# Optimization experiments

Hardware: AMD Instinct MI355X
Metric: run time of the kernel (lower is better)

The kernel has to match this reference:

```python
import jax, jax.numpy as jnp
import numpy as np

D_MODEL = 1024
NHEADS = 16
D_K = D_MODEL // NHEADS


def setup_inputs() -> dict:
    key = jax.random.key(0)
    ks = jax.random.split(key, 5)
    s = 1.0 / np.sqrt(D_MODEL)
    x = jax.random.normal(ks[0], (4, 2048, D_MODEL), dtype=jnp.float32)
    Wq = jax.random.normal(ks[1], (D_MODEL, D_MODEL), dtype=jnp.float32) * s
    Wk = jax.random.normal(ks[2], (D_MODEL, D_MODEL), dtype=jnp.float32) * s
    Wv = jax.random.normal(ks[3], (D_MODEL, D_MODEL), dtype=jnp.float32) * s
    Wo = jax.random.normal(ks[4], (D_MODEL, D_MODEL), dtype=jnp.float32) * s
    z = jnp.zeros((D_MODEL,), dtype=jnp.float32)
    return {"x": x, "Wq": Wq, "bq": z, "Wk": Wk, "bk": z,
            "Wv": Wv, "bv": z, "Wo": Wo, "bo": z}


def reference(x, Wq, bq, Wk, bk, Wv, bv, Wo, bo):
    B, S, _ = x.shape
    # nn.Linear: y = x @ W^T + b  (weights stored [out, in])
    def proj(W, b):
        h = x @ W.T + b                       # [B, S, D]
        return h.reshape(B, S, NHEADS, D_K).transpose(0, 2, 1, 3)  # [B, H, S, d_k]
    Q = proj(Wq, bq)
    K = proj(Wk, bk)
    V = proj(Wv, bv)
    scores = jnp.einsum("bhqd,bhkd->bhqk", Q, K) / jnp.sqrt(jnp.float32(D_K))
    attn = jax.nn.softmax(scores, axis=-1)    # dropout p=0.0 -> identity
    ctx = jnp.einsum("bhqk,bhkd->bhqd", attn, V)
    ctx = ctx.transpose(0, 2, 1, 3).reshape(B, S, D_MODEL)
    return ctx @ Wo.T + bo
```

## Files before the change

kernel.cpp:

```cpp
#include <hip/hip_runtime.h>
#include <stdint.h>
#include <stddef.h>

typedef _Float16 f16;
typedef f16 f16x8 __attribute__((ext_vector_type(8)));
typedef f16 f16x4 __attribute__((ext_vector_type(4)));
typedef f16 f16x2 __attribute__((ext_vector_type(2)));
typedef float f32x4 __attribute__((ext_vector_type(4)));
typedef float f32x16 __attribute__((ext_vector_type(16)));
typedef unsigned int u32x4 __attribute__((ext_vector_type(4)));

#define SEQ 2048
#define DM 1024
#define NH 16
#define DK 64
#define MTOT 8192

__device__ __forceinline__ void gload16(const f16* g, f16* l) {
    __builtin_amdgcn_global_load_lds(
        (const __attribute__((address_space(1))) uint32_t*)g,
        (__attribute__((address_space(3))) uint32_t*)l,
        16, 0, 0);
}

__device__ __forceinline__ unsigned int pkrtz(float a, float b) {
    return __builtin_bit_cast(unsigned int, __builtin_amdgcn_cvt_pkrtz(a, b));
}

__device__ __forceinline__ void plswap(unsigned int& a, unsigned int& b) {
    auto r = __builtin_amdgcn_permlane32_swap(a, b, false, false);
    unsigned int n0 = r[0], n1 = r[1];
    a = n0; b = n1;
}
__device__ __forceinline__ float xhalf_sum(float x) {
    unsigned int ux = __builtin_bit_cast(unsigned int, x);
    auto r = __builtin_amdgcn_permlane32_swap(ux, ux, false, false);
    unsigned int n0 = r[0], n1 = r[1];
    return __builtin_bit_cast(float, n0) + __builtin_bit_cast(float, n1);
}

__global__ void cvt_all(const float* __restrict__ x,
                        const float* __restrict__ w0, const float* __restrict__ w1,
                        const float* __restrict__ w2, const float* __restrict__ w3,
                        f16* __restrict__ xh,
                        f16* __restrict__ d0, f16* __restrict__ d1,
                        f16* __restrict__ d2, f16* __restrict__ d3) {
    int bid = blockIdx.x;
    const float* s;
    f16* d;
    int off;
    if (bid < 4096) { s = x; d = xh; off = bid; }
    else {
        int t = bid - 4096;
        int which = t >> 9;
        off = t & 511;
        s = which == 0 ? w0 : which == 1 ? w1 : which == 2 ? w2 : w3;
        d = which == 0 ? d0 : which == 1 ? d1 : which == 2 ? d2 : d3;
    }
    int i = (off * 256 + threadIdx.x) * 8;
    float4 a = *(const float4*)(s + i);
    float4 b = *(const float4*)(s + i + 4);
    f16x8 o = {(f16)a.x, (f16)a.y, (f16)a.z, (f16)a.w,
               (f16)b.x, (f16)b.y, (f16)b.z, (f16)b.w};
    *(f16x8*)(d + i) = o;
}

__device__ __forceinline__
void gemm_body(const f16* __restrict__ A, const f16* __restrict__ Bw,
               const float* __restrict__ bias, void* __restrict__ outp,
               int mode, float oscale, int bm, int bn, f16* As, f16* Bs) {
    const int tid = threadIdx.x;
    const int w = tid >> 6, lane = tid & 63;
    const int g = lane >> 4, c16 = lane & 15;
    const int wr = w >> 1, wc = w & 1;
    const int r8 = lane >> 3, co = (lane & 7) * 8;

    f32x4 acc[4][4] = {};

    const f16* Ab = A + (size_t)bm * 128 * DM;
    const f16* Bb = Bw + (size_t)bn * 128 * DM;

    for (int kt = 0; kt < DM / 64; ++kt) {
        if (kt) __syncthreads();
        const f16* As_src = Ab + kt * 64;
        const f16* Bs_src = Bb + kt * 64;
#pragma unroll
        for (int i = 0; i < 4; ++i) {
            int c = 4 * w + i;
            gload16(As_src + (size_t)(c * 8 + r8) * DM + co, As + c * 512);
            gload16(Bs_src + (size_t)(c * 8 + r8) * DM + co, Bs + c * 512);
        }
        __syncthreads();
#pragma unroll
        for (int kk = 0; kk < 2; ++kk) {
            f16x8 a[4], b[4];
            const int ko = kk * 32 + g * 8;
#pragma unroll
            for (int m = 0; m < 4; ++m)
                a[m] = *(const f16x8*)(As + (wr * 64 + m * 16 + c16) * 64 + ko);
#pragma unroll
            for (int n = 0; n < 4; ++n)
                b[n] = *(const f16x8*)(Bs + (wc * 64 + n * 16 + c16) * 64 + ko);
#pragma unroll
            for (int m = 0; m < 4; ++m)
#pragma unroll
                for (int n = 0; n < 4; ++n)
                    acc[m][n] = __builtin_amdgcn_mfma_f32_16x16x32_f16(a[m], b[n], acc[m][n], 0, 0, 0);
        }
    }

#pragma unroll
    for (int m = 0; m < 4; ++m) {
#pragma unroll
        for (int n = 0; n < 4; ++n) {
            const int col = bn * 128 + wc * 64 + n * 16 + c16;
            const float bv = bias[col];
            const int row0 = bm * 128 + wr * 64 + m * 16 + g * 4;
            if (mode == 1) {
                int b = row0 >> 11, s0 = row0 & 2047;
                int h = col >> 6, d = col & 63;
                f16x4 pv;
#pragma unroll
                for (int j = 0; j < 4; ++j) pv[j] = (f16)((acc[m][n][j] + bv) * oscale);
                *(f16x4*)((f16*)outp + (((size_t)(b * NH + h) * DK + d) * SEQ + s0)) = pv;
            } else if (mode == 0) {
#pragma unroll
                for (int j = 0; j < 4; ++j) {
                    int row = row0 + j;
                    int b = row >> 11, s = row & 2047;
                    int h = col >> 6, d = col & 63;
                    ((f16*)outp)[((size_t)(b * NH + h) * SEQ + s) * DK + d] =
                        (f16)((acc[m][n][j] + bv) * oscale);
                }
            } else {
#pragma unroll
                for (int j = 0; j < 4; ++j) {
                    int row = row0 + j;
                    ((float*)outp)[(size_t)row * DM + col] = acc[m][n][j] + bv;
                }
            }
        }
    }
}

__global__ __launch_bounds__(256, 2)
void gemm_qkv(const f16* __restrict__ A,
              const f16* __restrict__ W0, const f16* __restrict__ W1, const f16* __restrict__ W2,
              const float* __restrict__ b0, const float* __restrict__ b1, const float* __restrict__ b2,
              f16* __restrict__ Qo, f16* __restrict__ Ko, f16* __restrict__ Vto) {
    __shared__ __align__(16) f16 As[128 * 64];
    __shared__ __align__(16) f16 Bs[128 * 64];
    const int bid = blockIdx.x;
    const int wg = (bid & 7) * 192 + (bid >> 3);
    const int which = wg >> 9;
    const int t = wg & 511;
    const f16* Bw = which == 0 ? W0 : which == 1 ? W1 : W2;
    const float* bias = which == 0 ? b0 : which == 1 ? b1 : b2;
    void* outp = which == 0 ? (void*)Qo : which == 1 ? (void*)Ko : (void*)Vto;
    const int mode = (which == 2) ? 1 : 0;
    const float oscale = (which == 0) ? 0.18033688f : 1.0f;
    gemm_body(A, Bw, bias, outp, mode, oscale, t >> 3, t & 7, As, Bs);
}

__global__ __launch_bounds__(256, 2)
void gemm_out(const f16* __restrict__ A, const f16* __restrict__ Wo,
              const float* __restrict__ bias, float* __restrict__ outp) {
    __shared__ __align__(16) f16 As[128 * 64];
    __shared__ __align__(16) f16 Bs[128 * 64];
    const int bid = blockIdx.x;
    const int wg = (bid & 7) * 64 + (bid >> 3);
    gemm_body(A, Wo, bias, outp, 2, 1.0f, wg >> 3, wg & 7, As, Bs);
}

__global__ __launch_bounds__(512, 1)
void attn(const f16* __restrict__ Qg, const f16* __restrict__ Kg,
          const f16* __restrict__ Vg, f16* __restrict__ ctx) {
    __shared__ __align__(16) f16 SM[4][2][64 * 64];
    const int tid = threadIdx.x;
    const int w = tid >> 6, lane = tid & 63;
    const int q31 = lane & 31, hi = lane >> 5;
    const int bid = blockIdx.x;
    const int wg = (bid & 7) * 32 + (bid >> 3);
    const int bh = wg >> 2, qt = wg & 3;
    const int b = bh >> 4, h = bh & 15;
    const f16* Qp = Qg + (size_t)bh * SEQ * DK;
    const f16* Kp = Kg + (size_t)bh * SEQ * DK;
    const f16* Vp = Vg + (size_t)bh * DK * SEQ;
    const int q0w = qt * 512 + w * 64;

    f16x8 qfA[4], qfB[4];
#pragma unroll
    for (int ks4 = 0; ks4 < 4; ++ks4) {
        qfA[ks4] = *(const f16x8*)(Qp + (size_t)(q0w + q31) * DK + ks4 * 16 + hi * 8);
        qfB[ks4] = *(const f16x8*)(Qp + (size_t)(q0w + 32 + q31) * DK + ks4 * 16 + hi * 8);
    }

    const f32x16 z = {};
    const f16x2 one2 = {(f16)1.0f, (f16)1.0f};
    f32x16 OA0 = {}, OA1 = {}, OB0 = {}, OB1 = {};
    float lrA = 0.f, lrB = 0.f;

    const int srow = lane >> 3;
    const int scol = lane & 7;
    const int fsw = (q31 & 7) << 4;

#define STAGE(bufi, kvoff)                                                        \
    {                                                                             \
        int row_ = w * 8 + srow;                                                  \
        int csw_ = (scol ^ (row_ & 7)) * 8;                                       \
        gload16(Kp + (size_t)((kvoff) + row_) * DK + csw_, &SM[bufi][0][w * 512]); \
        gload16(Vp + (size_t)row_ * SEQ + (kvoff) + csw_, &SM[bufi][1][w * 512]);  \
    }

    auto qk = [&](const char* Kb, f32x16& A0, f32x16& A1, f32x16& B0, f32x16& B1) {
#pragma unroll
        for (int ks4 = 0; ks4 < 4; ++ks4) {
            const int off = (ks4 * 32 + hi * 16) ^ fsw;
            f16x8 kf0 = *(const f16x8*)(Kb + q31 * 128 + off);
            f16x8 kf1 = *(const f16x8*)(Kb + (32 + q31) * 128 + off);
            if (ks4 == 0) {
                A0 = __builtin_amdgcn_mfma_f32_32x32x16_f16(kf0, qfA[0], z, 0, 0, 0);
                B0 = __builtin_amdgcn_mfma_f32_32x32x16_f16(kf0, qfB[0], z, 0, 0, 0);
                A1 = __builtin_amdgcn_mfma_f32_32x32x16_f16(kf1, qfA[0], z, 0, 0, 0);
                B1 = __builtin_amdgcn_mfma_f32_32x32x16_f16(kf1, qfB[0], z, 0, 0, 0);
            } else {
                A0 = __builtin_amdgcn_mfma_f32_32x32x16_f16(kf0, qfA[ks4], A0, 0, 0, 0);
                B0 = __builtin_amdgcn_mfma_f32_32x32x16_f16(kf0, qfB[ks4], B0, 0, 0, 0);
                A1 = __builtin_amdgcn_mfma_f32_32x32x16_f16(kf1, qfA[ks4], A1, 0, 0, 0);
                B1 = __builtin_amdgcn_mfma_f32_32x32x16_f16(kf1, qfB[ks4], B1, 0, 0, 0);
            }
        }
    };

    auto pv = [&](const char* Vb, f16x8 (&pA)[4], f16x8 (&pB)[4]) {
#pragma unroll
        for (int ksl = 0; ksl < 4; ++ksl) {
            const int off = (ksl * 32 + hi * 16) ^ fsw;
            f16x8 vf0 = *(const f16x8*)(Vb + q31 * 128 + off);
            f16x8 vf1 = *(const f16x8*)(Vb + (32 + q31) * 128 + off);
            OA0 = __builtin_amdgcn_mfma_f32_32x32x16_f16(vf0, pA[ksl], OA0, 0, 0, 0);
            OA1 = __builtin_amdgcn_mfma_f32_32x32x16_f16(vf1, pA[ksl], OA1, 0, 0, 0);
            OB0 = __builtin_amdgcn_mfma_f32_32x32x16_f16(vf0, pB[ksl], OB0, 0, 0, 0);
            OB1 = __builtin_amdgcn_mfma_f32_32x32x16_f16(vf1, pB[ksl], OB1, 0, 0, 0);
        }
    };

    auto soft32 = [&](f32x16& sp, f16x8& paLo, f16x8& paHi, float& ls) {
#pragma unroll
        for (int r = 0; r < 16; ++r) sp[r] = __builtin_amdgcn_exp2f(sp[r]);
        unsigned int u[8];
#pragma unroll
        for (int j = 0; j < 4; ++j) {
            u[2 * j]     = pkrtz(sp[4 * j], sp[4 * j + 1]);
            u[2 * j + 1] = pkrtz(sp[4 * j + 2], sp[4 * j + 3]);
        }
        float ls0 = 0.f, ls1 = 0.f;
#pragma unroll
        for (int j = 0; j < 4; ++j) {
            ls0 = __builtin_amdgcn_fdot2(__builtin_bit_cast(f16x2, u[2 * j]), one2, ls0, false);
            ls1 = __builtin_amdgcn_fdot2(__builtin_bit_cast(f16x2, u[2 * j + 1]), one2, ls1, false);
        }
        ls += ls0 + ls1;
        plswap(u[0], u[2]);
        plswap(u[1], u[3]);
        plswap(u[4], u[6]);
        plswap(u[5], u[7]);
        u32x4 t0w = {u[0], u[1], u[2], u[3]};
        u32x4 t1w = {u[4], u[5], u[6], u[7]};
        paLo = __builtin_bit_cast(f16x8, t0w);
        paHi = __builtin_bit_cast(f16x8, t1w);
    };

    auto body = [&](int t, f16x8 (&pPA)[4], f16x8 (&pPB)[4],
                           f16x8 (&pCA)[4], f16x8 (&pCB)[4]) {
        if (t + 1 < 32) {
            asm volatile("s_waitcnt vmcnt(2)" ::: "memory");
        } else {
            asm volatile("s_waitcnt vmcnt(0)" ::: "memory");
        }
        __builtin_amdgcn_s_barrier();
        if (t + 2 < 32) STAGE((t + 2) & 3, (t + 2) * 64);

        const char* Kb = (const char*)&SM[t & 3][0][0];
        f32x16 sA0, sA1, sB0, sB1;
        if ((w >> 2) == 0) {
            qk(Kb, sA0, sA1, sB0, sB1);
            float lsA = 0.f, lsB = 0.f;
            soft32(sA0, pCA[0], pCA[1], lsA);
            soft32(sB0, pCB[0], pCB[1], lsB);
            soft32(sA1, pCA[2], pCA[3], lsA);
            soft32(sB1, pCB[2], pCB[3], lsB);
            lrA += lsA; lrB += lsB;
            pv((const char*)&SM[t & 3][1][0], pCA, pCB);
        } else {
            if (t > 0) pv((const char*)&SM[(t - 1) & 3][1][0], pPA, pPB);
            qk(Kb, sA0, sA1, sB0, sB1);
            float lsA = 0.f, lsB = 0.f;
            soft32(sA0, pCA[0], pCA[1], lsA);
            soft32(sB0, pCB[0], pCB[1], lsB);
            soft32(sA1, pCA[2], pCA[3], lsA);
            soft32(sB1, pCB[2], pCB[3], lsB);
            lrA += lsA; lrB += lsB;
        }
    };

    STAGE(0, 0);
    STAGE(1, 64);

    f16x8 paEA[4], paEB[4], paOA[4], paOB[4];
#pragma unroll
    for (int i = 0; i < 4; ++i) {
        paOA[i] = (f16x8){};
        paOB[i] = (f16x8){};
    }

    for (int t = 0; t < 32; t += 2) {
        body(t,     paOA, paOB, paEA, paEB);
        body(t + 1, paEA, paEB, paOA, paOB);
    }
    if ((w >> 2) != 0) {
        pv((const char*)&SM[3][1][0], paOA, paOB);
    }
#undef STAGE

    __syncthreads();

    f16* tw = &SM[0][0][0] + w * 4096;
    {
        const float rlA = 1.f / xhalf_sum(lrA);
        const float rlB = 1.f / xhalf_sum(lrB);
#pragma unroll
        for (int f = 0; f < 2; ++f) {
            const float rl = f ? rlB : rlA;
            char* twf = (char*)tw + f * 4096;
#pragma unroll
            for (int dblk = 0; dblk < 2; ++dblk) {
                const f32x16& Op = f ? (dblk ? OB1 : OB0) : (dblk ? OA1 : OA0);
#pragma unroll
                for (int rp = 0; rp < 8; ++rp) {
                    int r = 2 * rp;
                    int d0 = dblk * 32 + (r & 3) + 8 * (r >> 2) + 4 * hi;
                    unsigned int uv = pkrtz(Op[r] * rl, Op[r + 1] * rl);
                    *(unsigned int*)(twf + q31 * 128 + ((d0 * 2) ^ ((q31 & 7) << 4))) = uv;
                }
            }
        }
    }
#pragma unroll
    for (int p4 = 0; p4 < 8; ++p4) {
        int qq = p4 * 8 + (lane >> 3), ch = lane & 7;
        f16x8 v = *(const f16x8*)((const char*)tw + (qq >> 5) * 4096 + (qq & 31) * 128 +
                                  ((ch * 16) ^ ((qq & 7) << 4)));
        *(f16x8*)(ctx + (size_t)(b * SEQ + q0w + qq) * DM + h * DK + ch * 8) = v;
    }
}

extern "C" void kernel_launch(void* const* d_in, const int* in_sizes, int n_in,
                              void* d_out, int out_size, void* d_ws, size_t ws_size,
                              hipStream_t stream) {
    const float* x  = (const float*)d_in[0];
    const float* Wq = (const float*)d_in[1];
    const float* bq = (const float*)d_in[2];
    const float* Wk = (const float*)d_in[3];
    const float* bk = (const float*)d_in[4];
    const float* Wv = (const float*)d_in[5];
    const float* bv = (const float*)d_in[6];
    const float* Wo = (const float*)d_in[7];
    const float* bo = (const float*)d_in[8];

    f16* ws  = (f16*)d_ws;
    f16* xh  = ws;
    f16* Wqh = ws + (size_t)8 * 1024 * 1024;
    f16* Wkh = Wqh + 1024 * 1024;
    f16* Wvh = Wkh + 1024 * 1024;
    f16* Woh = Wvh + 1024 * 1024;
    f16* Vtb = Woh + 1024 * 1024;
    f16* Qb = (f16*)d_out;
    f16* Kb = Qb + (size_t)8 * 1024 * 1024;
    f16* ctx = xh;

    cvt_all<<<4096 + 4 * 512, 256, 0, stream>>>(x, Wq, Wk, Wv, Wo, xh, Wqh, Wkh, Wvh, Woh);

    gemm_qkv<<<1536, 256, 0, stream>>>(xh, Wqh, Wkh, Wvh, bq, bk, bv, Qb, Kb, Vtb);

    attn<<<256, 512, 0, stream>>>(Qb, Kb, Vtb, ctx);

    gemm_out<<<512, 256, 0, stream>>>(ctx, Woh, bo, (float*)d_out);
}
```

Before: 184.9 us.

## Replace QKV GEMM with 256x256 tile double-buffered 8-wave kernel

Replaces the 128x128-tile QKV projection GEMM with a 256x256-tile, 512-thread kernel. The kernel double-buffers LDS with async global-to-LDS loads, uses XOR swizzling to avoid bank conflicts, and interleaves the next tile's loads with MFMA phases under s_setprio. The aim is more operand reuse per tile and load latency hidden behind compute. The cost is 128KB of LDS per block, which may limit occupancy to one block per CU. With only 384 blocks the grid may also leave CUs unevenly loaded. The shared gemm_body is reduced to the fp32 output path used by the output projection.

```diff
diff --git a/kernel.cpp b/kernel.cpp
--- a/kernel.cpp
+++ b/kernel.cpp
@@ -65,10 +65,137 @@
     *(f16x8*)(d + i) = o;
 }
 
+__global__ __launch_bounds__(512, 2)
+void gemm_qkv8(const f16* __restrict__ A,
+               const f16* __restrict__ W0, const f16* __restrict__ W1, const f16* __restrict__ W2,
+               const float* __restrict__ b0, const float* __restrict__ b1, const float* __restrict__ b2,
+               f16* __restrict__ Qo, f16* __restrict__ Ko, f16* __restrict__ Vto) {
+    __shared__ __align__(16) f16 Asl[2][2][128 * 64];
+    __shared__ __align__(16) f16 Bsl[2][2][128 * 64];
+    const int tid = threadIdx.x;
+    const int w = tid >> 6, lane = tid & 63;
+    const int g = lane >> 4, c16 = lane & 15;
+    const int wr = w >> 2, wc = w & 3;
+    const int srow = lane >> 3, scol = lane & 7;
+    const int bid = blockIdx.x;
+    const int wg = (bid & 7) * 48 + (bid >> 3);
+    const int bm = wg / 12, bn = wg % 12;
+    const int which = bn >> 2, bnm = bn & 3;
+    const f16* Bw = which == 0 ? W0 : which == 1 ? W1 : W2;
+    const float* bias = which == 0 ? b0 : which == 1 ? b1 : b2;
+    const float oscale = (which == 0) ? 0.18033688f : 1.0f;
+    const int mode = (which == 2) ? 1 : 0;
+    void* outp = which == 0 ? (void*)Qo : which == 1 ? (void*)Ko : (void*)Vto;
+
+    const f16* Ab = A + (size_t)bm * 256 * DM;
+    const f16* Bb = Bw + (size_t)bnm * 256 * DM;
+    const int csw = (scol ^ srow) * 8;
+
+#define STAGE_A(slot, half, kt)                                                     \
+    {                                                                               \
+        _Pragma("unroll")                                                           \
+        for (int i_ = 0; i_ < 2; ++i_) {                                            \
+            int row_ = (half) * 128 + i_ * 64 + w * 8 + srow;                       \
+            gload16(Ab + (size_t)row_ * DM + (kt) * 64 + csw,                       \
+                    &Asl[slot][half][(i_ * 64 + w * 8) * 64]);                      \
+        }                                                                           \
+    }
+#define STAGE_B(slot, half, kt)                                                     \
+    {                                                                               \
+        _Pragma("unroll")                                                           \
+        for (int i_ = 0; i_ < 2; ++i_) {                                            \
+            int row_ = (half) * 128 + i_ * 64 + w * 8 + srow;                       \
+            gload16(Bb + (size_t)row_ * DM + (kt) * 64 + csw,                       \
+                    &Bsl[slot][half][(i_ * 64 + w * 8) * 64]);                      \
+        }                                                                           \
+    }
+
+    f32x4 acc[8][4] = {};
+    f16x8 bfr[4];
+    const int rsw = (c16 & 7) << 4;
+
+    STAGE_A(0, 0, 0); STAGE_A(0, 1, 0); STAGE_B(0, 0, 0); STAGE_B(0, 1, 0);
+
+    for (int kt = 0; kt < 16; ++kt) {
+        const int slot = kt & 1, nslot = slot ^ 1;
+        asm volatile("s_waitcnt vmcnt(0)" ::: "memory");
+        __builtin_amdgcn_s_barrier();
+
+        const char* Ah = (const char*)&Asl[slot][wr][0];
+        const char* Bh = (const char*)&Bsl[slot][wc >> 1][0];
+        const int brow0 = (wc & 1) * 64;
+
+#pragma unroll
+        for (int p = 0; p < 4; ++p) {
+            const int mh = p & 1, kk = p >> 1;
+            const int ko = (kk * 64 + g * 16);
+            f16x8 afr[4];
+#pragma unroll
+            for (int mi = 0; mi < 4; ++mi) {
+                int row = mh * 64 + mi * 16 + c16;
+                afr[mi] = *(const f16x8*)(Ah + row * 128 + (ko ^ rsw));
+            }
+            if (mh == 0) {
+#pragma unroll
+                for (int ni = 0; ni < 4; ++ni) {
+                    int row = brow0 + ni * 16 + c16;
+                    bfr[ni] = *(const f16x8*)(Bh + row * 128 + (ko ^ rsw));
+                }
+            }
+            if (kt + 1 < 16) {
+                if (p == 0)      STAGE_A(nslot, 0, kt + 1)
+                else if (p == 1) STAGE_A(nslot, 1, kt + 1)
+                else if (p == 2) STAGE_B(nslot, 0, kt + 1)
+                else             STAGE_B(nslot, 1, kt + 1)
+            }
+            __builtin_amdgcn_s_barrier();
+            __builtin_amdgcn_s_setprio(1);
+#pragma unroll
+            for (int mi = 0; mi < 4; ++mi)
+#pragma unroll
+                for (int ni = 0; ni < 4; ++ni)
+                    acc[mh * 4 + mi][ni] =
+                        __builtin_amdgcn_mfma_f32_16x16x32_f16(afr[mi], bfr[ni],
+                                                               acc[mh * 4 + mi][ni], 0, 0, 0);
+            __builtin_amdgcn_s_setprio(0);
+            __builtin_amdgcn_s_barrier();
+        }
+    }
+#undef STAGE_A
+#undef STAGE_B
+
+#pragma unroll
+    for (int mi = 0; mi < 8; ++mi) {
+#pragma unroll
+        for (int ni = 0; ni < 4; ++ni) {
+            const int col = bnm * 256 + wc * 64 + ni * 16 + c16;
+            const float bv = bias[col];
+            const int row0 = bm * 256 + wr * 128 + mi * 16 + g * 4;
+            if (mode == 1) {
+                int b = row0 >> 11, s0 = row0 & 2047;
+                int h = col >> 6, d = col & 63;
+                f16x4 pv;
+#pragma unroll
+                for (int j = 0; j < 4; ++j) pv[j] = (f16)((acc[mi][ni][j] + bv));
+                *(f16x4*)((f16*)outp + (((size_t)(b * NH + h) * DK + d) * SEQ + s0)) = pv;
+            } else {
+#pragma unroll
+                for (int j = 0; j < 4; ++j) {
+                    int row = row0 + j;
+                    int b = row >> 11, s = row & 2047;
+                    int h = col >> 6, d = col & 63;
+                    ((f16*)outp)[((size_t)(b * NH + h) * SEQ + s) * DK + d] =
+                        (f16)((acc[mi][ni][j] + bv) * oscale);
+                }
+            }
+        }
+    }
+}
+
 __device__ __forceinline__
 void gemm_body(const f16* __restrict__ A, const f16* __restrict__ Bw,
-               const float* __restrict__ bias, void* __restrict__ outp,
-               int mode, float oscale, int bm, int bn, f16* As, f16* Bs) {
+               const float* __restrict__ bias, float* __restrict__ outp,
+               int bm, int bn, f16* As, f16* Bs) {
     const int tid = threadIdx.x;
     const int w = tid >> 6, lane = tid & 63;
     const int g = lane >> 4, c16 = lane & 15;
@@ -116,50 +243,13 @@
             const int col = bn * 128 + wc * 64 + n * 16 + c16;
             const float bv = bias[col];
             const int row0 = bm * 128 + wr * 64 + m * 16 + g * 4;
-            if (mode == 1) {
-                int b = row0 >> 11, s0 = row0 & 2047;
-                int h = col >> 6, d = col & 63;
-                f16x4 pv;
-#pragma unroll
-                for (int j = 0; j < 4; ++j) pv[j] = (f16)((acc[m][n][j] + bv) * oscale);
-                *(f16x4*)((f16*)outp + (((size_t)(b * NH + h) * DK + d) * SEQ + s0)) = pv;
-            } else if (mode == 0) {
-#pragma unroll
-                for (int j = 0; j < 4; ++j) {
-                    int row = row0 + j;
-                    int b = row >> 11, s = row & 2047;
-                    int h = col >> 6, d = col & 63;
-                    ((f16*)outp)[((size_t)(b * NH + h) * SEQ + s) * DK + d] =
-                        (f16)((acc[m][n][j] + bv) * oscale);
-                }
-            } else {
-#pragma unroll
-                for (int j = 0; j < 4; ++j) {
-                    int row = row0 + j;
-                    ((float*)outp)[(size_t)row * DM + col] = acc[m][n][j] + bv;
-                }
-            }
-        }
-    }
-}
-
-__global__ __launch_bounds__(256, 2)
-void gemm_qkv(const f16* __restrict__ A,
-              const f16* __restrict__ W0, const f16* __restrict__ W1, const f16* __restrict__ W2,
-              const float* __restrict__ b0, const float* __restrict__ b1, const float* __restrict__ b2,
-              f16* __restrict__ Qo, f16* __restrict__ Ko, f16* __restrict__ Vto) {
-    __shared__ __align__(16) f16 As[128 * 64];
-    __shared__ __align__(16) f16 Bs[128 * 64];
-    const int bid = blockIdx.x;
-    const int wg = (bid & 7) * 192 + (bid >> 3);
-    const int which = wg >> 9;
-    const int t = wg & 511;
-    const f16* Bw = which == 0 ? W0 : which == 1 ? W1 : W2;
-    const float* bias = which == 0 ? b0 : which == 1 ? b1 : b2;
-    void* outp = which == 0 ? (void*)Qo : which == 1 ? (void*)Ko : (void*)Vto;
-    const int mode = (which == 2) ? 1 : 0;
-    const float oscale = (which == 0) ? 0.18033688f : 1.0f;
-    gemm_body(A, Bw, bias, outp, mode, oscale, t >> 3, t & 7, As, Bs);
+#pragma unroll
+            for (int j = 0; j < 4; ++j) {
+                int row = row0 + j;
+                outp[(size_t)row * DM + col] = acc[m][n][j] + bv;
+            }
+        }
+    }
 }
 
 __global__ __launch_bounds__(256, 2)
@@ -169,7 +259,7 @@
     __shared__ __align__(16) f16 Bs[128 * 64];
     const int bid = blockIdx.x;
     const int wg = (bid & 7) * 64 + (bid >> 3);
-    gemm_body(A, Wo, bias, outp, 2, 1.0f, wg >> 3, wg & 7, As, Bs);
+    gemm_body(A, Wo, bias, outp, wg >> 3, wg & 7, As, Bs);
 }
 
 __global__ __launch_bounds__(512, 1)
@@ -381,7 +471,7 @@
 
     cvt_all<<<4096 + 4 * 512, 256, 0, stream>>>(x, Wq, Wk, Wv, Wo, xh, Wqh, Wkh, Wvh, Woh);
 
-    gemm_qkv<<<1536, 256, 0, stream>>>(xh, Wqh, Wkh, Wvh, bq, bk, bv, Qb, Kb, Vtb);
+    gemm_qkv8<<<384, 512, 0, stream>>>(xh, Wqh, Wkh, Wvh, bq, bk, bv, Qb, Kb, Vtb);
 
     attn<<<256, 512, 0, stream>>>(Qb, Kb, Vtb, ctx);
 
```

After: 185.9 us. About the same (+0.6%).

## Use 256x128 double-buffered swizzled-LDS GEMM tiles with 8 waves for projections

Applied to the files above, without the earlier changes.

Replaces the 128x128 single-buffered GEMM body with a 256x128 tile run by 512 threads. The next K-slice is prefetched into a second LDS buffer while MFMAs run on the current one, and the prefetch is split across the two inner k-steps. The LDS layout is XOR-swizzled to avoid bank conflicts on fragment reads, and s_setprio is raised around the MFMA blocks. This targets load-latency stalls and LDS conflicts, at the cost of more LDS per block, one block per CU, and fewer blocks in the grid.

```diff
diff --git a/kernel.cpp b/kernel.cpp
--- a/kernel.cpp
+++ b/kernel.cpp
@@ -66,62 +66,78 @@
 }
 
 __device__ __forceinline__
-void gemm_body(const f16* __restrict__ A, const f16* __restrict__ Bw,
-               const float* __restrict__ bias, void* __restrict__ outp,
-               int mode, float oscale, int bm, int bn, f16* As, f16* Bs) {
+void gemm256_body(const f16* __restrict__ Ab, const f16* __restrict__ Bb,
+                  const float* __restrict__ bias, void* __restrict__ outp,
+                  int mode, float oscale, int bm, int colbase,
+                  f16* Asl, f16* Bsl) {
     const int tid = threadIdx.x;
     const int w = tid >> 6, lane = tid & 63;
     const int g = lane >> 4, c16 = lane & 15;
     const int wr = w >> 1, wc = w & 1;
-    const int r8 = lane >> 3, co = (lane & 7) * 8;
+    const int srow = lane >> 3, scol = lane & 7;
+    const int csw = (scol ^ srow) * 8;
+    const int rsw = (c16 & 7) << 4;
 
     f32x4 acc[4][4] = {};
 
-    const f16* Ab = A + (size_t)bm * 128 * DM;
-    const f16* Bb = Bw + (size_t)bn * 128 * DM;
-
-    for (int kt = 0; kt < DM / 64; ++kt) {
-        if (kt) __syncthreads();
-        const f16* As_src = Ab + kt * 64;
-        const f16* Bs_src = Bb + kt * 64;
-#pragma unroll
-        for (int i = 0; i < 4; ++i) {
-            int c = 4 * w + i;
-            gload16(As_src + (size_t)(c * 8 + r8) * DM + co, As + c * 512);
-            gload16(Bs_src + (size_t)(c * 8 + r8) * DM + co, Bs + c * 512);
-        }
-        __syncthreads();
-#pragma unroll
-        for (int kk = 0; kk < 2; ++kk) {
-            f16x8 a[4], b[4];
-            const int ko = kk * 32 + g * 8;
-#pragma unroll
-            for (int m = 0; m < 4; ++m)
-                a[m] = *(const f16x8*)(As + (wr * 64 + m * 16 + c16) * 64 + ko);
-#pragma unroll
-            for (int n = 0; n < 4; ++n)
-                b[n] = *(const f16x8*)(Bs + (wc * 64 + n * 16 + c16) * 64 + ko);
-#pragma unroll
-            for (int m = 0; m < 4; ++m)
-#pragma unroll
-                for (int n = 0; n < 4; ++n)
-                    acc[m][n] = __builtin_amdgcn_mfma_f32_16x16x32_f16(a[m], b[n], acc[m][n], 0, 0, 0);
-        }
-    }
-
-#pragma unroll
-    for (int m = 0; m < 4; ++m) {
-#pragma unroll
-        for (int n = 0; n < 4; ++n) {
-            const int col = bn * 128 + wc * 64 + n * 16 + c16;
+#define SA(slot, i_, kt) gload16(Ab + (size_t)((w * 4 + (i_)) * 8 + srow) * DM + (kt) * 64 + csw, \
+                                 Asl + (slot) * 16384 + (w * 4 + (i_)) * 512)
+#define SB(slot, i_, kt) gload16(Bb + (size_t)((w * 2 + (i_)) * 8 + srow) * DM + (kt) * 64 + csw, \
+                                 Bsl + (slot) * 8192 + (w * 2 + (i_)) * 512)
+
+    SA(0, 0, 0); SA(0, 1, 0); SA(0, 2, 0); SA(0, 3, 0); SB(0, 0, 0); SB(0, 1, 0);
+
+    for (int kt = 0; kt < 16; ++kt) {
+        const int slot = kt & 1, ns = slot ^ 1;
+        asm volatile("s_waitcnt vmcnt(0)" ::: "memory");
+        __builtin_amdgcn_s_barrier();
+        const char* Ah = (const char*)(Asl + slot * 16384);
+        const char* Bh = (const char*)(Bsl + slot * 8192);
+#pragma unroll
+        for (int p = 0; p < 2; ++p) {
+            f16x8 afr[4], bfr[4];
+            const int ko = p * 64 + g * 16;
+#pragma unroll
+            for (int mi = 0; mi < 4; ++mi) {
+                int row = wr * 64 + mi * 16 + c16;
+                afr[mi] = *(const f16x8*)(Ah + row * 128 + (ko ^ rsw));
+            }
+#pragma unroll
+            for (int ni = 0; ni < 4; ++ni) {
+                int row = wc * 64 + ni * 16 + c16;
+                bfr[ni] = *(const f16x8*)(Bh + row * 128 + (ko ^ rsw));
+            }
+            if (kt + 1 < 16) {
+                if (p == 0) { SA(ns, 0, kt + 1); SA(ns, 1, kt + 1); SB(ns, 0, kt + 1); }
+                else        { SA(ns, 2, kt + 1); SA(ns, 3, kt + 1); SB(ns, 1, kt + 1); }
+            }
+            __builtin_amdgcn_s_barrier();
+            __builtin_amdgcn_s_setprio(1);
+#pragma unroll
+            for (int mi = 0; mi < 4; ++mi)
+#pragma unroll
+                for (int ni = 0; ni < 4; ++ni)
+                    acc[mi][ni] = __builtin_amdgcn_mfma_f32_16x16x32_f16(
+                        afr[mi], bfr[ni], acc[mi][ni], 0, 0, 0);
+            __builtin_amdgcn_s_setprio(0);
+        }
+    }
+#undef SA
+#undef SB
+
+#pragma unroll
+    for (int mi = 0; mi < 4; ++mi) {
+#pragma unroll
+        for (int ni = 0; ni < 4; ++ni) {
+            const int col = colbase + wc * 64 + ni * 16 + c16;
             const float bv = bias[col];
-            const int row0 = bm * 128 + wr * 64 + m * 16 + g * 4;
+            const int row0 = bm * 256 + wr * 64 + mi * 16 + g * 4;
             if (mode == 1) {
                 int b = row0 >> 11, s0 = row0 & 2047;
                 int h = col >> 6, d = col & 63;
                 f16x4 pv;
 #pragma unroll
-                for (int j = 0; j < 4; ++j) pv[j] = (f16)((acc[m][n][j] + bv) * oscale);
+                for (int j = 0; j < 4; ++j) pv[j] = (f16)(acc[mi][ni][j] + bv);
                 *(f16x4*)((f16*)outp + (((size_t)(b * NH + h) * DK + d) * SEQ + s0)) = pv;
             } else if (mode == 0) {
 #pragma unroll
@@ -130,46 +146,49 @@
                     int b = row >> 11, s = row & 2047;
                     int h = col >> 6, d = col & 63;
                     ((f16*)outp)[((size_t)(b * NH + h) * SEQ + s) * DK + d] =
-                        (f16)((acc[m][n][j] + bv) * oscale);
+                        (f16)((acc[mi][ni][j] + bv) * oscale);
                 }
             } else {
 #pragma unroll
                 for (int j = 0; j < 4; ++j) {
                     int row = row0 + j;
-                    ((float*)outp)[(size_t)row * DM + col] = acc[m][n][j] + bv;
+                    ((float*)outp)[(size_t)row * DM + col] = acc[mi][ni][j] + bv;
                 }
             }
         }
     }
 }
 
-__global__ __launch_bounds__(256, 2)
-void gemm_qkv(const f16* __restrict__ A,
-              const f16* __restrict__ W0, const f16* __restrict__ W1, const f16* __restrict__ W2,
-              const float* __restrict__ b0, const float* __restrict__ b1, const float* __restrict__ b2,
-              f16* __restrict__ Qo, f16* __restrict__ Ko, f16* __restrict__ Vto) {
-    __shared__ __align__(16) f16 As[128 * 64];
-    __shared__ __align__(16) f16 Bs[128 * 64];
+__global__ __launch_bounds__(512, 1)
+void gemm_qkv8(const f16* __restrict__ A,
+               const f16* __restrict__ W0, const f16* __restrict__ W1, const f16* __restrict__ W2,
+               const float* __restrict__ b0, const float* __restrict__ b1, const float* __restrict__ b2,
+               f16* __restrict__ Qo, f16* __restrict__ Ko, f16* __restrict__ Vto) {
+    __shared__ __align__(16) f16 Asl[2 * 256 * 64];
+    __shared__ __align__(16) f16 Bsl[2 * 128 * 64];
     const int bid = blockIdx.x;
-    const int wg = (bid & 7) * 192 + (bid >> 3);
-    const int which = wg >> 9;
-    const int t = wg & 511;
+    const int wg = (bid & 7) * 96 + (bid >> 3);
+    const int bm = wg / 24, bn = wg % 24;
+    const int which = bn >> 3, bnm = bn & 7;
     const f16* Bw = which == 0 ? W0 : which == 1 ? W1 : W2;
     const float* bias = which == 0 ? b0 : which == 1 ? b1 : b2;
+    const float oscale = (which == 0) ? 0.18033688f : 1.0f;
+    const int mode = (which == 2) ? 1 : 0;
     void* outp = which == 0 ? (void*)Qo : which == 1 ? (void*)Ko : (void*)Vto;
-    const int mode = (which == 2) ? 1 : 0;
-    const float oscale = (which == 0) ? 0.18033688f : 1.0f;
-    gemm_body(A, Bw, bias, outp, mode, oscale, t >> 3, t & 7, As, Bs);
-}
-
-__global__ __launch_bounds__(256, 2)
-void gemm_out(const f16* __restrict__ A, const f16* __restrict__ Wo,
-              const float* __restrict__ bias, float* __restrict__ outp) {
-    __shared__ __align__(16) f16 As[128 * 64];
-    __shared__ __align__(16) f16 Bs[128 * 64];
+    gemm256_body(A + (size_t)bm * 256 * DM, Bw + (size_t)bnm * 128 * DM,
+                 bias, outp, mode, oscale, bm, bnm * 128, Asl, Bsl);
+}
+
+__global__ __launch_bounds__(512, 1)
+void gemm_out8(const f16* __restrict__ A, const f16* __restrict__ Wo,
+               const float* __restrict__ bias, float* __restrict__ outp) {
+    __shared__ __align__(16) f16 Asl[2 * 256 * 64];
+    __shared__ __align__(16) f16 Bsl[2 * 128 * 64];
     const int bid = blockIdx.x;
-    const int wg = (bid & 7) * 64 + (bid >> 3);
-    gemm_body(A, Wo, bias, outp, 2, 1.0f, wg >> 3, wg & 7, As, Bs);
+    const int wg = (bid & 7) * 32 + (bid >> 3);
+    const int bm = wg >> 3, bn = wg & 7;
+    gemm256_body(A + (size_t)bm * 256 * DM, Wo + (size_t)bn * 128 * DM,
+                 bias, (void*)outp, 2, 1.0f, bm, bn * 128, Asl, Bsl);
 }
 
 __global__ __launch_bounds__(512, 1)
@@ -381,9 +400,9 @@
 
     cvt_all<<<4096 + 4 * 512, 256, 0, stream>>>(x, Wq, Wk, Wv, Wo, xh, Wqh, Wkh, Wvh, Woh);
 
-    gemm_qkv<<<1536, 256, 0, stream>>>(xh, Wqh, Wkh, Wvh, bq, bk, bv, Qb, Kb, Vtb);
+    gemm_qkv8<<<768, 512, 0, stream>>>(xh, Wqh, Wkh, Wvh, bq, bk, bv, Qb, Kb, Vtb);
 
     attn<<<256, 512, 0, stream>>>(Qb, Kb, Vtb, ctx);
 
-    gemm_out<<<512, 256, 0, stream>>>(ctx, Woh, bo, (float*)d_out);
-}
+    gemm_out8<<<256, 512, 0, stream>>>(ctx, Woh, bo, (float*)d_out);
+}
```

New measurement: 177.5 us. 4.0% less time.
